# Performance work log

Hardware: AMD Instinct MI355X
Metric: run time of the kernel (lower is better)

## Reference

```python
import jax, jax.numpy as jnp
import numpy as np

N = 50000
E = 800000
D = 16            # input_dim == hidden_dim == output_dim (required for consistency)
D2 = D * D
HEADS = 4
NEG_SLOPE = 0.2


def _gat_conv(x, src, dst, W, att_src, att_dst, bias):
    """PyG GATConv with concat=False (mean over heads), add_self_loops already applied.
    x: [N, Cin], W: [Cin, H*C], att_*: [H, C], bias: [C]."""
    H, C = att_src.shape
    xh = (x @ W).reshape(N, H, C)                     # [N, H, C]
    a_src = jnp.einsum('nhc,hc->nh', xh, att_src)      # [N, H]
    a_dst = jnp.einsum('nhc,hc->nh', xh, att_dst)
    alpha = jax.nn.leaky_relu(a_src[src] + a_dst[dst], NEG_SLOPE)   # [E, H]
    amax = jax.ops.segment_max(alpha, dst, num_segments=N)
    amax = jnp.where(jnp.isfinite(amax), amax, 0.0)
    ex = jnp.exp(alpha - jax.lax.stop_gradient(amax)[dst])
    denom = jax.ops.segment_sum(ex, dst, num_segments=N)
    coef = ex / (denom[dst] + 1e-16)                  # per-dst softmax over incoming edges
    acc = jnp.zeros((N, C), x.dtype)
    for h in range(H):  # loop over heads to avoid [E, H, C] intermediate
        acc = acc + jax.ops.segment_sum(coef[:, h:h + 1] * xh[src, h], dst, num_segments=N)
    return acc / H + bias


def setup_inputs() -> dict:
    key = jax.random.key(0)
    ks = jax.random.split(key, 20)
    s = lambda k, shape, fan: jax.random.normal(k, shape, jnp.float32) * (1.0 / np.sqrt(fan))
    inp = {
        'mean': jax.random.normal(ks[0], (N, D), jnp.float32),
        'cov': jax.random.normal(ks[1], (N, D, D), jnp.float32),
        'edge_index': jax.random.randint(ks[2], (2, E), 0, N, jnp.int32),
        # gat_mean params
        'W_mean': s(ks[3], (D, HEADS * D), D),
        'att_src_mean': s(ks[4], (HEADS, D), D),
        'att_dst_mean': s(ks[5], (HEADS, D), D),
        'bias_mean': jnp.zeros((D,), jnp.float32),
        # gat_cov params
        'W_cov': s(ks[6], (D2, HEADS * D2), D2),
        'att_src_cov': s(ks[7], (HEADS, D2), D2),
        'att_dst_cov': s(ks[8], (HEADS, D2), D2),
        'bias_cov': jnp.zeros((D2,), jnp.float32),
        # fc_mean: Linear(D,D) -> Linear(D,D)
        'fm_W1': s(ks[9], (D, D), D), 'fm_b1': jnp.zeros((D,), jnp.float32),
        'fm_W2': s(ks[10], (D, D), D), 'fm_b2': jnp.zeros((D,), jnp.float32),
        # fc_cov: Linear(D2,D2) -> Linear(D2,D2)
        'fcv_W1': s(ks[11], (D2, D2), D2), 'fcv_b1': jnp.zeros((D2,), jnp.float32),
        'fcv_W2': s(ks[12], (D2, D2), D2), 'fcv_b2': jnp.zeros((D2,), jnp.float32),
    }
    return inp


def reference(mean, cov, edge_index, W_mean, att_src_mean, att_dst_mean, bias_mean,
              W_cov, att_src_cov, att_dst_cov, bias_cov,
              fm_W1, fm_b1, fm_W2, fm_b2, fcv_W1, fcv_b1, fcv_W2, fcv_b2):
    loops = jnp.arange(N, dtype=edge_index.dtype)
    src = jnp.concatenate([edge_index[0], loops])
    dst = jnp.concatenate([edge_index[1], loops])

    cov_flat = cov.reshape(N, D2)
    mean_agg = _gat_conv(mean, src, dst, W_mean, att_src_mean, att_dst_mean, bias_mean)
    cov_agg = _gat_conv(cov_flat, src, dst, W_cov, att_src_cov, att_dst_cov, bias_cov)

    mean_out = (mean_agg @ fm_W1 + fm_b1) @ fm_W2 + fm_b2
    cov_out = (cov_agg @ fcv_W1 + fcv_b1) @ fcv_W2 + fcv_b2
    return mean_out, cov_out.reshape(N, D, D)
```

## Files before the change

kernel.cpp:

```cpp
#include <hip/hip_runtime.h>

#define NN 50000
#define EE 800000
#define DD 16
#define DD2 256
#define ETOT (EE + NN)
#define NB 196

typedef __bf16 bf16x8 __attribute__((ext_vector_type(8)));
typedef float f32x4 __attribute__((ext_vector_type(4)));
typedef float f32x2 __attribute__((ext_vector_type(2)));

__device__ inline unsigned short f2bf(float f) {
    unsigned int u = __float_as_uint(f);
    return (unsigned short)((u + 0x7FFFu + ((u >> 16) & 1u)) >> 16);
}

__device__ inline void gl2lds16(const void* g, void* l) {
    __builtin_amdgcn_global_load_lds((const __attribute__((address_space(1))) unsigned int*)g,
                                     (__attribute__((address_space(3))) unsigned int*)l, 16, 0, 0);
}

__global__ void k_count(const int* ei, int* counts) {
    int e = blockIdx.x * 256 + threadIdx.x;
    if (e < EE) atomicAdd(&counts[ei[EE + e]], 1);
}

__global__ void k_scan1(const int* counts, int* partial, int* bsum) {
    __shared__ int sh[256];
    int t = threadIdx.x;
    int n = blockIdx.x * 256 + t;
    int v = (n < NN) ? counts[n] + 1 : 0;
    sh[t] = v;
    __syncthreads();
    for (int d = 1; d < 256; d <<= 1) {
        int x = (t >= d) ? sh[t - d] : 0;
        __syncthreads();
        sh[t] += x;
        __syncthreads();
    }
    if (n < NN) partial[n] = sh[t];
    if (t == 255) bsum[blockIdx.x] = sh[255];
}

__global__ void k_scan3(const int* counts, const int* partial, const int* bsum,
                        int* row_start, int* cursor) {
    __shared__ int sh[256];
    int t = threadIdx.x;
    int v = (t < NB) ? bsum[t] : 0;
    sh[t] = v;
    __syncthreads();
    for (int d = 1; d < 256; d <<= 1) {
        int x = (t >= d) ? sh[t - d] : 0;
        __syncthreads();
        sh[t] += x;
        __syncthreads();
    }
    int boff = (blockIdx.x == 0) ? 0 : sh[blockIdx.x - 1];
    int n = blockIdx.x * 256 + t;
    if (n < NN) {
        int rs = partial[n] - (counts[n] + 1) + boff;
        row_start[n] = rs;
        cursor[n] = rs;
        if (n == NN - 1) row_start[NN] = partial[n] + boff;
    }
}

__global__ void k_scatter(const int* ei, int* cursor, int* srt) {
    int i = blockIdx.x * 256 + threadIdx.x;
    if (i >= ETOT) return;
    int s, d;
    if (i < EE) { s = ei[i]; d = ei[EE + i]; }
    else { s = d = i - EE; }
    int pos = atomicAdd(&cursor[d], 1);
    srt[pos] = s;
}

__global__ void k_pre(const float* fcv_W1, const float* fcv_W2, const float* fcv_b1, const float* fcv_b2,
                      const float* fm_W1, const float* fm_W2, const float* fm_b1, const float* fm_b2,
                      const float* W_cov, const float* as_cov, const float* ad_cov,
                      const float* W_mean, const float* as_mean, const float* ad_mean,
                      const float* bias_cov, const float* bias_mean,
                      unsigned short* WpT, float* bpc, float* vcov, float* vmean,
                      float* Wpm, float* bpm) {
    __shared__ float sh[256];
    int b = blockIdx.x, t = threadIdx.x;
    if (b < 1024) {
        int q = b >> 8, i = b & 255;
        const float* wrow = W_cov + (size_t)i * 1024 + q * 256;
        float t1 = 0.f;
        for (int j = 0; j < 256; ++j) t1 += wrow[j] * fcv_W1[j * 256 + t];
        sh[t] = t1;
        __syncthreads();
        float s = 0.f;
        for (int k = 0; k < 256; ++k) s += sh[k] * fcv_W2[k * 256 + t];
        int C = q * 32 + (i >> 3);
        int cs = C ^ (t & 7);
        WpT[(size_t)t * 1024 + cs * 8 + (i & 7)] = f2bf(0.25f * s);
    } else if (b == 1024) {
        float t1 = fcv_b1[t];
        for (int j = 0; j < 256; ++j) t1 += bias_cov[j] * fcv_W1[j * 256 + t];
        sh[t] = t1;
        __syncthreads();
        float s = fcv_b2[t];
        for (int k = 0; k < 256; ++k) s += sh[k] * fcv_W2[k * 256 + t];
        bpc[t] = s;
    } else if (b < 1033) {
        int ch = b - 1025, h = ch & 3;
        const float* att = (ch < 4) ? as_cov : ad_cov;
        int jl = t & 31, i8 = t >> 5;
        float av[8];
#pragma unroll
        for (int jj = 0; jj < 8; ++jj) av[jj] = att[h * 256 + jj * 32 + jl];
        for (int ii = 0; ii < 32; ++ii) {
            int i = ii * 8 + i8;
            const float* wr = W_cov + (size_t)i * 1024 + h * 256;
            float p = 0.f;
#pragma unroll
            for (int jj = 0; jj < 8; ++jj) p += wr[jj * 32 + jl] * av[jj];
#pragma unroll
            for (int off = 16; off; off >>= 1) p += __shfl_xor(p, off);
            if (jl == 0) vcov[ch * 256 + i] = p;
        }
    } else {
        {
            int j = t >> 4, c = t & 15;
            float s = 0.f;
            for (int k = 0; k < 16; ++k) s += fm_W1[j * 16 + k] * fm_W2[k * 16 + c];
            sh[j * 16 + c] = s;
        }
        if (t < 128) {
            int ch = t >> 4, i = t & 15, h = ch & 3;
            const float* att = (ch < 4) ? as_mean : ad_mean;
            float s = 0.f;
            for (int j = 0; j < 16; ++j) s += W_mean[i * 64 + h * 16 + j] * att[h * 16 + j];
            vmean[ch * 16 + i] = s;
        }
        __syncthreads();
#pragma unroll
        for (int r = 0; r < 4; ++r) {
            int idx = r * 256 + t;
            int k = idx >> 4, c = idx & 15, h = k >> 4, i = k & 15;
            float s = 0.f;
            for (int j = 0; j < 16; ++j) s += W_mean[i * 64 + h * 16 + j] * sh[j * 16 + c];
            Wpm[k * 16 + c] = 0.25f * s;
        }
        if (t < 16) {
            float b2 = fm_b2[t];
            for (int k = 0; k < 16; ++k) b2 += fm_b1[k] * fm_W2[k * 16 + t];
            float s = b2;
            for (int j = 0; j < 16; ++j) s += bias_mean[j] * sh[j * 16 + t];
            bpm[t] = s;
        }
    }
}

__global__ void __launch_bounds__(256) k_dots(const float* cov, const float* mean,
                                              const float* vcov, const float* vmean,
                                              float* asrc, float* adst, unsigned short* covb) {
    __shared__ float vc[8 * 256];
    __shared__ float vm[8 * 16];
    int t = threadIdx.x;
    for (int i = t; i < 2048; i += 256) vc[i] = vcov[i];
    if (t < 128) vm[t] = vmean[t];
    __syncthreads();
    int w = t >> 6, lane = t & 63;
    int n = blockIdx.x * 4 + w;
    float4 x = *(const float4*)(cov + (size_t)n * 256 + lane * 4);
    unsigned int u0 = (unsigned int)f2bf(x.x) | ((unsigned int)f2bf(x.y) << 16);
    unsigned int u1 = (unsigned int)f2bf(x.z) | ((unsigned int)f2bf(x.w) << 16);
    *(uint2*)((char*)covb + (size_t)n * 512 + lane * 8) = make_uint2(u0, u1);
    float p[8];
#pragma unroll
    for (int c = 0; c < 8; ++c) {
        float4 v = *(const float4*)&vc[c * 256 + lane * 4];
        p[c] = x.x * v.x + x.y * v.y + x.z * v.z + x.w * v.w;
    }
#pragma unroll
    for (int c = 0; c < 8; ++c)
        for (int off = 32; off; off >>= 1) p[c] += __shfl_xor(p[c], off);
    float xm = (lane < 16) ? mean[(size_t)n * 16 + lane] : 0.f;
    float q[8];
#pragma unroll
    for (int c = 0; c < 8; ++c) {
        q[c] = (lane < 16) ? xm * vm[c * 16 + lane] : 0.f;
        for (int off = 8; off; off >>= 1) q[c] += __shfl_xor(q[c], off);
    }
    if (lane == 0) {
        float4* ps = (float4*)(asrc + (size_t)n * 8);
        ps[0] = make_float4(p[0], p[1], p[2], p[3]);
        ps[1] = make_float4(q[0], q[1], q[2], q[3]);
        float4* pd = (float4*)(adst + (size_t)n * 8);
        pd[0] = make_float4(p[4], p[5], p[6], p[7]);
        pd[1] = make_float4(q[4], q[5], q[6], q[7]);
    }
}

__global__ void __launch_bounds__(256) k_agg(const int* row_start, const int* srt,
                                             const float* asrc, const float* adst,
                                             const unsigned short* covb, const float* mean,
                                             unsigned short* Ycat, float* Ym) {
    __shared__ float exbuf[4][64][8];
    int t = threadIdx.x;
    int w = t >> 6, lane = t & 63;
    int n = blockIdx.x * 4 + w;
    int beg = row_start[n], deg = row_start[n + 1] - beg;
    int ml = lane & 15;
    float ad[8];
    {
        const float4* pd = (const float4*)(adst + (size_t)n * 8);
        float4 d0 = pd[0], d1 = pd[1];
        ad[0] = d0.x; ad[1] = d0.y; ad[2] = d0.z; ad[3] = d0.w;
        ad[4] = d1.x; ad[5] = d1.y; ad[6] = d1.z; ad[7] = d1.w;
    }
    f32x2 acc[8];
#pragma unroll
    for (int k = 0; k < 8; ++k) acc[k] = (f32x2){0.f, 0.f};
    float accm[4] = {0, 0, 0, 0};
    float ds8[8] = {0, 0, 0, 0, 0, 0, 0, 0};

    for (int base = 0; base < deg; base += 64) {
        int i = base + lane;
        bool valid = i < deg;
        int s0 = srt[beg + (valid ? i : (deg - 1))];
        const float4* pa = (const float4*)(asrc + (size_t)s0 * 8);
        float4 a0 = pa[0], a1 = pa[1];
        float av[8] = {a0.x, a0.y, a0.z, a0.w, a1.x, a1.y, a1.z, a1.w};
        float ex8[8];
#pragma unroll
        for (int c = 0; c < 8; ++c) {
            float al = av[c] + ad[c];
            al = (al >= 0.f) ? al : 0.2f * al;
            float e = __expf(al);
            e = valid ? e : 0.f;
            ex8[c] = e;
            ds8[c] += e;
        }
        *(float4*)&exbuf[w][lane][0] = make_float4(ex8[0], ex8[1], ex8[2], ex8[3]);
        *(float4*)&exbuf[w][lane][4] = make_float4(ex8[4], ex8[5], ex8[6], ex8[7]);
        int cnt = min(64, deg - base);
        int cnt4 = (cnt + 3) & ~3;
        for (int jp = 0; jp < cnt4; jp += 4) {
            int se[4];
            float4 e0[4], e1[4];
#pragma unroll
            for (int k = 0; k < 4; ++k) se[k] = __shfl(s0, jp + k);
#pragma unroll
            for (int k = 0; k < 4; ++k) {
                e0[k] = *(const float4*)&exbuf[w][jp + k][0];
                e1[k] = *(const float4*)&exbuf[w][jp + k][4];
            }
            uint2 cd[4];
            float mv[4];
#pragma unroll
            for (int k = 0; k < 4; ++k) {
                cd[k] = *(const uint2*)((const char*)covb + (size_t)se[k] * 512 + lane * 8);
                mv[k] = mean[(size_t)se[k] * 16 + ml];
            }
#pragma unroll
            for (int k = 0; k < 4; ++k) {
                f32x2 x0 = (f32x2){__uint_as_float(cd[k].x << 16), __uint_as_float(cd[k].x & 0xffff0000u)};
                f32x2 x1 = (f32x2){__uint_as_float(cd[k].y << 16), __uint_as_float(cd[k].y & 0xffff0000u)};
                float ev[4] = {e0[k].x, e0[k].y, e0[k].z, e0[k].w};
#pragma unroll
                for (int h = 0; h < 4; ++h) {
                    f32x2 e2 = (f32x2){ev[h], ev[h]};
                    acc[h * 2 + 0] = __builtin_elementwise_fma(e2, x0, acc[h * 2 + 0]);
                    acc[h * 2 + 1] = __builtin_elementwise_fma(e2, x1, acc[h * 2 + 1]);
                }
                accm[0] += e1[k].x * mv[k]; accm[1] += e1[k].y * mv[k];
                accm[2] += e1[k].z * mv[k]; accm[3] += e1[k].w * mv[k];
            }
        }
    }
#pragma unroll
    for (int c = 0; c < 8; ++c)
        for (int off = 32; off; off >>= 1) ds8[c] += __shfl_xor(ds8[c], off);

    float invc[4] = {1.f / (ds8[0] + 1e-16f), 1.f / (ds8[1] + 1e-16f),
                     1.f / (ds8[2] + 1e-16f), 1.f / (ds8[3] + 1e-16f)};
    float invm[4] = {1.f / (ds8[4] + 1e-16f), 1.f / (ds8[5] + 1e-16f),
                     1.f / (ds8[6] + 1e-16f), 1.f / (ds8[7] + 1e-16f)};
    char* yrow = (char*)Ycat + (size_t)n * 2048;
    int cbase = lane >> 1, hl = lane & 1, sw = n & 7;
#pragma unroll
    for (int h = 0; h < 4; ++h) {
        float iv = invc[h];
        uint2 pk;
        pk.x = (unsigned int)f2bf(acc[h * 2 + 0].x * iv) | ((unsigned int)f2bf(acc[h * 2 + 0].y * iv) << 16);
        pk.y = (unsigned int)f2bf(acc[h * 2 + 1].x * iv) | ((unsigned int)f2bf(acc[h * 2 + 1].y * iv) << 16);
        int cs = (h * 32 + cbase) ^ sw;
        *(uint2*)(yrow + cs * 16 + hl * 8) = pk;
    }
    if (lane < 16) {
#pragma unroll
        for (int h = 0; h < 4; ++h) Ym[(size_t)n * 64 + h * 16 + lane] = accm[h] * invm[h];
    }
}

__global__ void __launch_bounds__(256) k_gemm(const unsigned short* Ycat, const unsigned short* WpT,
                                              const float* bpc, float* out_cov,
                                              const float* Ym, const float* Wpm, const float* bpm,
                                              float* out_mean) {
    __shared__ __align__(16) unsigned short As[128 * 64];
    __shared__ __align__(16) unsigned short Bs[128 * 64];
    int t = threadIdx.x;
    if (blockIdx.x >= 782) {
        float* wm = (float*)As;
        float* bmv = (float*)Bs;
        for (int i = t; i < 1024; i += 256) wm[i] = Wpm[i];
        if (t < 16) bmv[t] = bpm[t];
        __syncthreads();
        int base = (blockIdx.x - 782) * 256;
        int c = t & 15;
#pragma unroll
        for (int p = 0; p < 16; ++p) {
            int node = base + p * 16 + (t >> 4);
            if (node < NN) {
                const float* yr = Ym + (size_t)node * 64;
                float s = bmv[c];
#pragma unroll
                for (int k = 0; k < 64; ++k) s += yr[k] * wm[k * 16 + c];
                out_mean[(size_t)node * 16 + c] = s;
            }
        }
        return;
    }
    int m0 = (blockIdx.x >> 1) * 128, c0 = (blockIdx.x & 1) * 128;
    int w = t >> 6, lane = t & 63;
    int mg = w >> 1, ng = w & 1;
    int q = lane >> 4, lm = lane & 15;
    f32x4 acc[4][4];
#pragma unroll
    for (int mt = 0; mt < 4; ++mt)
#pragma unroll
        for (int nt = 0; nt < 4; ++nt) acc[mt][nt] = (f32x4){0.f, 0.f, 0.f, 0.f};

    for (int kc = 0; kc < 16; ++kc) {
        int k0 = kc * 64;
#pragma unroll
        for (int i2 = 0; i2 < 4; ++i2) {
            int idx = t + i2 * 256;
            int row = idx >> 3, seg = idx & 7;
            int gm = m0 + row;
            if (gm < NN)
                gl2lds16(Ycat + (size_t)gm * 1024 + k0 + seg * 8, As + idx * 8);
        }
#pragma unroll
        for (int i2 = 0; i2 < 4; ++i2) {
            int idx = t + i2 * 256;
            int col = idx >> 3, seg = idx & 7;
            gl2lds16(WpT + (size_t)(c0 + col) * 1024 + k0 + seg * 8, Bs + idx * 8);
        }
        __syncthreads();
#pragma unroll
        for (int ks = 0; ks < 2; ++ks) {
            bf16x8 af[4], bfr[4];
#pragma unroll
            for (int mt = 0; mt < 4; ++mt) {
                int row = mg * 64 + mt * 16 + lm;
                int ch = (ks * 4 + q) ^ (row & 7);
                af[mt] = *(const bf16x8*)(As + row * 64 + ch * 8);
            }
#pragma unroll
            for (int nt = 0; nt < 4; ++nt) {
                int col = ng * 64 + nt * 16 + lm;
                int ch = (ks * 4 + q) ^ (col & 7);
                bfr[nt] = *(const bf16x8*)(Bs + col * 64 + ch * 8);
            }
#pragma unroll
            for (int mt = 0; mt < 4; ++mt)
#pragma unroll
                for (int nt = 0; nt < 4; ++nt)
                    acc[mt][nt] = __builtin_amdgcn_mfma_f32_16x16x32_bf16(af[mt], bfr[nt], acc[mt][nt], 0, 0, 0);
        }
        __syncthreads();
    }
#pragma unroll
    for (int nt = 0; nt < 4; ++nt) {
        int col = c0 + ng * 64 + nt * 16 + lm;
        float bias = bpc[col];
#pragma unroll
        for (int mt = 0; mt < 4; ++mt) {
#pragma unroll
            for (int e = 0; e < 4; ++e) {
                int r = m0 + mg * 64 + mt * 16 + q * 4 + e;
                if (r < NN)
                    __builtin_nontemporal_store(acc[mt][nt][e] + bias, &out_cov[(size_t)r * 256 + col]);
            }
        }
    }
}

extern "C" void kernel_launch(void* const* d_in, const int* in_sizes, int n_in,
                              void* d_out, int out_size, void* d_ws, size_t ws_size,
                              hipStream_t stream) {
    const float* mean = (const float*)d_in[0];
    const float* cov = (const float*)d_in[1];
    const int* ei = (const int*)d_in[2];
    const float* W_mean = (const float*)d_in[3];
    const float* as_mean = (const float*)d_in[4];
    const float* ad_mean = (const float*)d_in[5];
    const float* bias_mean = (const float*)d_in[6];
    const float* W_cov = (const float*)d_in[7];
    const float* as_cov = (const float*)d_in[8];
    const float* ad_cov = (const float*)d_in[9];
    const float* bias_cov = (const float*)d_in[10];
    const float* fm_W1 = (const float*)d_in[11];
    const float* fm_b1 = (const float*)d_in[12];
    const float* fm_W2 = (const float*)d_in[13];
    const float* fm_b2 = (const float*)d_in[14];
    const float* fcv_W1 = (const float*)d_in[15];
    const float* fcv_b1 = (const float*)d_in[16];
    const float* fcv_W2 = (const float*)d_in[17];
    const float* fcv_b2 = (const float*)d_in[18];

    float* out_mean = (float*)d_out;
    float* out_cov = (float*)d_out + (size_t)NN * DD;

    char* w = (char*)d_ws;
    auto alloc = [&](size_t bytes) -> void* {
        void* p = (void*)w;
        w += (bytes + 255) & ~(size_t)255;
        return p;
    };
    unsigned short* Ycat = (unsigned short*)alloc((size_t)NN * 1024 * 2);
    unsigned short* covb = (unsigned short*)alloc((size_t)NN * 256 * 2);
    float* Ym = (float*)alloc((size_t)NN * 64 * 4);
    int* counts = (int*)alloc(NN * 4);
    int* partial = (int*)alloc(NN * 4);
    int* bsum = (int*)alloc(256 * 4);
    int* row_start = (int*)alloc((NN + 1) * 4);
    int* cursor = (int*)alloc(NN * 4);
    int* srt = (int*)alloc((size_t)ETOT * 4);
    float* asrc = (float*)alloc((size_t)NN * 8 * 4);
    float* adst = (float*)alloc((size_t)NN * 8 * 4);
    float* vcov = (float*)alloc(8 * 256 * 4);
    float* vmean = (float*)alloc(8 * 16 * 4);
    unsigned short* WpT = (unsigned short*)alloc(256 * 1024 * 2);
    float* bpc = (float*)alloc(256 * 4);
    float* Wpm = (float*)alloc(64 * 16 * 4);
    float* bpm = (float*)alloc(16 * 4);

    hipMemsetAsync(counts, 0, NN * 4, stream);
    k_count<<<(EE + 255) / 256, 256, 0, stream>>>(ei, counts);
    k_scan1<<<NB, 256, 0, stream>>>(counts, partial, bsum);
    k_scan3<<<NB, 256, 0, stream>>>(counts, partial, bsum, row_start, cursor);
    k_scatter<<<(ETOT + 255) / 256, 256, 0, stream>>>(ei, cursor, srt);
    k_pre<<<1034, 256, 0, stream>>>(fcv_W1, fcv_W2, fcv_b1, fcv_b2, fm_W1, fm_W2, fm_b1, fm_b2,
                                    W_cov, as_cov, ad_cov, W_mean, as_mean, ad_mean,
                                    bias_cov, bias_mean, WpT, bpc, vcov, vmean, Wpm, bpm);
    k_dots<<<NN / 4, 256, 0, stream>>>(cov, mean, vcov, vmean, asrc, adst, covb);
    k_agg<<<NN / 4, 256, 0, stream>>>(row_start, srt, asrc, adst, covb, mean, Ycat, Ym);
    k_gemm<<<782 + 196, 256, 0, stream>>>(Ycat, WpT, bpc, out_cov, Ym, Wpm, bpm, out_mean);
}
```

Measured before the change: 456.4 us.

## Software-pipeline neighbor gathers in aggregation kernel with persistent grid-stride blocks

The aggregation kernel now runs as a persistent grid of 2048 blocks that stride over destination nodes, instead of one block per four nodes. Inside the edge loop it double-buffers the cov/mean gathers, issuing the next group's loads before computing the current group, so memory latency is hidden. It also spreads the mean-head accumulation across all 64 lanes, one head per 16-lane group, removing redundant work, and uses 32-bit offset arithmetic plus __restrict__ qualifiers. The trade-offs are higher register pressure from the second set of buffers and possible load imbalance across the strided nodes.

```diff
diff --git a/kernel.cpp b/kernel.cpp
--- a/kernel.cpp
+++ b/kernel.cpp
@@ -196,105 +196,119 @@
     }
 }
 
-__global__ void __launch_bounds__(256) k_agg(const int* row_start, const int* srt,
-                                             const float* asrc, const float* adst,
-                                             const unsigned short* covb, const float* mean,
-                                             unsigned short* Ycat, float* Ym) {
+__global__ void __launch_bounds__(256) k_agg(const int* __restrict__ row_start, const int* __restrict__ srt,
+                                             const float* __restrict__ asrc, const float* __restrict__ adst,
+                                             const unsigned short* __restrict__ covb, const float* __restrict__ mean,
+                                             unsigned short* __restrict__ Ycat, float* __restrict__ Ym) {
     __shared__ float exbuf[4][64][8];
     int t = threadIdx.x;
     int w = t >> 6, lane = t & 63;
-    int n = blockIdx.x * 4 + w;
-    int beg = row_start[n], deg = row_start[n + 1] - beg;
     int ml = lane & 15;
-    float ad[8];
-    {
-        const float4* pd = (const float4*)(adst + (size_t)n * 8);
-        float4 d0 = pd[0], d1 = pd[1];
-        ad[0] = d0.x; ad[1] = d0.y; ad[2] = d0.z; ad[3] = d0.w;
-        ad[4] = d1.x; ad[5] = d1.y; ad[6] = d1.z; ad[7] = d1.w;
-    }
-    f32x2 acc[8];
-#pragma unroll
-    for (int k = 0; k < 8; ++k) acc[k] = (f32x2){0.f, 0.f};
-    float accm[4] = {0, 0, 0, 0};
-    float ds8[8] = {0, 0, 0, 0, 0, 0, 0, 0};
-
-    for (int base = 0; base < deg; base += 64) {
-        int i = base + lane;
-        bool valid = i < deg;
-        int s0 = srt[beg + (valid ? i : (deg - 1))];
-        const float4* pa = (const float4*)(asrc + (size_t)s0 * 8);
-        float4 a0 = pa[0], a1 = pa[1];
-        float av[8] = {a0.x, a0.y, a0.z, a0.w, a1.x, a1.y, a1.z, a1.w};
-        float ex8[8];
-#pragma unroll
-        for (int c = 0; c < 8; ++c) {
-            float al = av[c] + ad[c];
-            al = (al >= 0.f) ? al : 0.2f * al;
-            float e = __expf(al);
-            e = valid ? e : 0.f;
-            ex8[c] = e;
-            ds8[c] += e;
-        }
-        *(float4*)&exbuf[w][lane][0] = make_float4(ex8[0], ex8[1], ex8[2], ex8[3]);
-        *(float4*)&exbuf[w][lane][4] = make_float4(ex8[4], ex8[5], ex8[6], ex8[7]);
-        int cnt = min(64, deg - base);
-        int cnt4 = (cnt + 3) & ~3;
-        for (int jp = 0; jp < cnt4; jp += 4) {
+    int hl4 = lane >> 4;
+    const char* covbc = (const char*)covb;
+    const char* meanc = (const char*)mean;
+    const char* asrcc = (const char*)asrc;
+    unsigned lodc = (unsigned)lane << 3;
+    unsigned lodm = (unsigned)ml << 2;
+
+    for (int n = blockIdx.x * 4 + w; n < NN; n += gridDim.x * 4) {
+        int beg = row_start[n], deg = row_start[n + 1] - beg;
+        float ad[8];
+        {
+            const float4* pd = (const float4*)(adst + (size_t)n * 8);
+            float4 d0 = pd[0], d1 = pd[1];
+            ad[0] = d0.x; ad[1] = d0.y; ad[2] = d0.z; ad[3] = d0.w;
+            ad[4] = d1.x; ad[5] = d1.y; ad[6] = d1.z; ad[7] = d1.w;
+        }
+        f32x2 acc[8];
+#pragma unroll
+        for (int k = 0; k < 8; ++k) acc[k] = (f32x2){0.f, 0.f};
+        float accm = 0.f;
+        float ds8[8] = {0, 0, 0, 0, 0, 0, 0, 0};
+
+        auto loadg = [&](int jp, int s0v, uint2* cd, float* mv) {
             int se[4];
-            float4 e0[4], e1[4];
-#pragma unroll
-            for (int k = 0; k < 4; ++k) se[k] = __shfl(s0, jp + k);
-#pragma unroll
-            for (int k = 0; k < 4; ++k) {
-                e0[k] = *(const float4*)&exbuf[w][jp + k][0];
-                e1[k] = *(const float4*)&exbuf[w][jp + k][4];
-            }
-            uint2 cd[4];
-            float mv[4];
-#pragma unroll
-            for (int k = 0; k < 4; ++k) {
-                cd[k] = *(const uint2*)((const char*)covb + (size_t)se[k] * 512 + lane * 8);
-                mv[k] = mean[(size_t)se[k] * 16 + ml];
-            }
-#pragma unroll
-            for (int k = 0; k < 4; ++k) {
-                f32x2 x0 = (f32x2){__uint_as_float(cd[k].x << 16), __uint_as_float(cd[k].x & 0xffff0000u)};
-                f32x2 x1 = (f32x2){__uint_as_float(cd[k].y << 16), __uint_as_float(cd[k].y & 0xffff0000u)};
-                float ev[4] = {e0[k].x, e0[k].y, e0[k].z, e0[k].w};
+#pragma unroll
+            for (int k2 = 0; k2 < 4; ++k2) se[k2] = __shfl(s0v, jp + k2);
+#pragma unroll
+            for (int k2 = 0; k2 < 4; ++k2) {
+                cd[k2] = *(const uint2*)(covbc + (((unsigned)se[k2] << 9) + lodc));
+                mv[k2] = *(const float*)(meanc + (((unsigned)se[k2] << 6) + lodm));
+            }
+        };
+        auto compute4 = [&](int jp, const uint2* cd, const float* mv) {
+#pragma unroll
+            for (int k2 = 0; k2 < 4; ++k2) {
+                float4 e0 = *(const float4*)&exbuf[w][jp + k2][0];
+                float em = exbuf[w][jp + k2][4 + hl4];
+                f32x2 x0 = (f32x2){__uint_as_float(cd[k2].x << 16), __uint_as_float(cd[k2].x & 0xffff0000u)};
+                f32x2 x1 = (f32x2){__uint_as_float(cd[k2].y << 16), __uint_as_float(cd[k2].y & 0xffff0000u)};
+                float ev[4] = {e0.x, e0.y, e0.z, e0.w};
 #pragma unroll
                 for (int h = 0; h < 4; ++h) {
                     f32x2 e2 = (f32x2){ev[h], ev[h]};
                     acc[h * 2 + 0] = __builtin_elementwise_fma(e2, x0, acc[h * 2 + 0]);
                     acc[h * 2 + 1] = __builtin_elementwise_fma(e2, x1, acc[h * 2 + 1]);
                 }
-                accm[0] += e1[k].x * mv[k]; accm[1] += e1[k].y * mv[k];
-                accm[2] += e1[k].z * mv[k]; accm[3] += e1[k].w * mv[k];
-            }
-        }
-    }
-#pragma unroll
-    for (int c = 0; c < 8; ++c)
-        for (int off = 32; off; off >>= 1) ds8[c] += __shfl_xor(ds8[c], off);
-
-    float invc[4] = {1.f / (ds8[0] + 1e-16f), 1.f / (ds8[1] + 1e-16f),
-                     1.f / (ds8[2] + 1e-16f), 1.f / (ds8[3] + 1e-16f)};
-    float invm[4] = {1.f / (ds8[4] + 1e-16f), 1.f / (ds8[5] + 1e-16f),
-                     1.f / (ds8[6] + 1e-16f), 1.f / (ds8[7] + 1e-16f)};
-    char* yrow = (char*)Ycat + (size_t)n * 2048;
-    int cbase = lane >> 1, hl = lane & 1, sw = n & 7;
-#pragma unroll
-    for (int h = 0; h < 4; ++h) {
-        float iv = invc[h];
-        uint2 pk;
-        pk.x = (unsigned int)f2bf(acc[h * 2 + 0].x * iv) | ((unsigned int)f2bf(acc[h * 2 + 0].y * iv) << 16);
-        pk.y = (unsigned int)f2bf(acc[h * 2 + 1].x * iv) | ((unsigned int)f2bf(acc[h * 2 + 1].y * iv) << 16);
-        int cs = (h * 32 + cbase) ^ sw;
-        *(uint2*)(yrow + cs * 16 + hl * 8) = pk;
-    }
-    if (lane < 16) {
-#pragma unroll
-        for (int h = 0; h < 4; ++h) Ym[(size_t)n * 64 + h * 16 + lane] = accm[h] * invm[h];
+                accm += em * mv[k2];
+            }
+        };
+
+        for (int base = 0; base < deg; base += 64) {
+            int i = base + lane;
+            bool valid = i < deg;
+            int s0 = srt[beg + (valid ? i : (deg - 1))];
+            int cnt = min(64, deg - base);
+            int cnt4 = (cnt + 3) & ~3;
+
+            uint2 cdA[4], cdB[4];
+            float mvA[4], mvB[4];
+            loadg(0, s0, cdA, mvA);
+
+            const float4* pa = (const float4*)(asrcc + ((size_t)((unsigned)s0 << 5)));
+            float4 a0 = pa[0], a1 = pa[1];
+            float av[8] = {a0.x, a0.y, a0.z, a0.w, a1.x, a1.y, a1.z, a1.w};
+            float ex8[8];
+#pragma unroll
+            for (int c = 0; c < 8; ++c) {
+                float al = av[c] + ad[c];
+                al = (al >= 0.f) ? al : 0.2f * al;
+                float e = __expf(al);
+                e = valid ? e : 0.f;
+                ex8[c] = e;
+                ds8[c] += e;
+            }
+            *(float4*)&exbuf[w][lane][0] = make_float4(ex8[0], ex8[1], ex8[2], ex8[3]);
+            *(float4*)&exbuf[w][lane][4] = make_float4(ex8[4], ex8[5], ex8[6], ex8[7]);
+
+            for (int jp = 0; jp < cnt4; jp += 8) {
+                bool hasB = (jp + 4) < cnt4;
+                if (hasB) loadg(jp + 4, s0, cdB, mvB);
+                compute4(jp, cdA, mvA);
+                if (jp + 8 < cnt4) loadg(jp + 8, s0, cdA, mvA);
+                if (hasB) compute4(jp + 4, cdB, mvB);
+            }
+        }
+#pragma unroll
+        for (int c = 0; c < 8; ++c)
+            for (int off = 32; off; off >>= 1) ds8[c] += __shfl_xor(ds8[c], off);
+
+        float invc[4] = {1.f / (ds8[0] + 1e-16f), 1.f / (ds8[1] + 1e-16f),
+                         1.f / (ds8[2] + 1e-16f), 1.f / (ds8[3] + 1e-16f)};
+        float dsm = (hl4 == 0) ? ds8[4] : (hl4 == 1) ? ds8[5] : (hl4 == 2) ? ds8[6] : ds8[7];
+        float invm = 1.f / (dsm + 1e-16f);
+        char* yrow = (char*)Ycat + (size_t)n * 2048;
+        int cbase = lane >> 1, hl = lane & 1, sw = n & 7;
+#pragma unroll
+        for (int h = 0; h < 4; ++h) {
+            float iv = invc[h];
+            uint2 pk;
+            pk.x = (unsigned int)f2bf(acc[h * 2 + 0].x * iv) | ((unsigned int)f2bf(acc[h * 2 + 0].y * iv) << 16);
+            pk.y = (unsigned int)f2bf(acc[h * 2 + 1].x * iv) | ((unsigned int)f2bf(acc[h * 2 + 1].y * iv) << 16);
+            int cs = (h * 32 + cbase) ^ sw;
+            *(uint2*)(yrow + cs * 16 + hl * 8) = pk;
+        }
+        Ym[(size_t)n * 64 + lane] = accm * invm;
     }
 }
 
@@ -451,6 +465,6 @@
                                     W_cov, as_cov, ad_cov, W_mean, as_mean, ad_mean,
                                     bias_cov, bias_mean, WpT, bpc, vcov, vmean, Wpm, bpm);
     k_dots<<<NN / 4, 256, 0, stream>>>(cov, mean, vcov, vmean, asrc, adst, covb);
-    k_agg<<<NN / 4, 256, 0, stream>>>(row_start, srt, asrc, adst, covb, mean, Ycat, Ym);
+    k_agg<<<2048, 256, 0, stream>>>(row_start, srt, asrc, adst, covb, mean, Ycat, Ym);
     k_gemm<<<782 + 196, 256, 0, stream>>>(Ycat, WpT, bpc, out_cov, Ym, Wpm, bpm, out_mean);
 }
```

Measured after the change: 459.0 us. No clear change (+0.6%).
